# Kernel tuning notes

Hardware: AMD Instinct MI355X
Metric: run time of the kernel (lower is better)

## Reference

```python
import jax, jax.numpy as jnp
import numpy as np

# Mamba2(d_model=256, headdim=32) defaults: d_state=128, d_conv=4, expand=2, ngroups=1, chunk=256
B, CIN, L = 8, 256, 1024
D_MODEL = CIN
D_INNER = 2 * D_MODEL            # expand=2 -> 512
HEADDIM = 32
NHEADS = D_INNER // HEADDIM      # 16
D_STATE = 128
D_CONV = 4
CONV_DIM = D_INNER + 2 * D_STATE             # 768 (ngroups=1)
D_IN_PROJ = 2 * D_INNER + 2 * D_STATE + NHEADS  # 1296
GN_GROUPS = 8
CHUNK = 256
EPS = 1e-5

def setup_inputs():
    key = jax.random.key(0)
    ks = jax.random.split(key, 8)
    x = jax.random.normal(ks[0], (B, CIN, L), jnp.float32)
    W_in = jax.random.normal(ks[1], (D_IN_PROJ, D_MODEL), jnp.float32) * 0.02
    conv_w = jax.random.normal(ks[2], (CONV_DIM, D_CONV), jnp.float32) * 0.2
    conv_b = jax.random.normal(ks[3], (CONV_DIM,), jnp.float32) * 0.02
    dt = jnp.exp(jax.random.uniform(ks[4], (NHEADS,)) * (jnp.log(0.1) - jnp.log(0.001)) + jnp.log(0.001))
    dt_bias = dt + jnp.log(-jnp.expm1(-dt))   # inverse softplus
    A_log = jnp.log(jax.random.uniform(ks[5], (NHEADS,), minval=1.0, maxval=16.0))
    Dp = jnp.ones((NHEADS,), jnp.float32)
    rms_w = jnp.ones((D_INNER,), jnp.float32)
    W_out = jax.random.normal(ks[6], (D_MODEL, D_INNER), jnp.float32) * 0.02
    gn_w = jnp.ones((CIN,), jnp.float32)
    gn_b = jnp.zeros((CIN,), jnp.float32)
    return dict(x=x, W_in=W_in, conv_w=conv_w, conv_b=conv_b, dt_bias=dt_bias,
                A_log=A_log, Dp=Dp, rms_w=rms_w, W_out=W_out, gn_w=gn_w, gn_b=gn_b)

def segsum(a):
    # a: (..., T) -> (..., T, T) with sum_{j<i<=t} a_i on/below diagonal, -inf above
    T = a.shape[-1]
    cs = jnp.cumsum(a, -1)
    d = cs[..., :, None] - cs[..., None, :]
    mask = jnp.tril(jnp.ones((T, T), bool))
    return jnp.where(mask, d, -jnp.inf)

def ssd(X, A, Bm, Cm):
    # X: (b,l,h,p) already dt-scaled; A: (b,l,h) = dt*A_cont; Bm,Cm: (b,l,n) (ngroups=1)
    b, l, h, p = X.shape
    n = Bm.shape[-1]
    c = l // CHUNK
    X = X.reshape(b, c, CHUNK, h, p)
    A = A.reshape(b, c, CHUNK, h).transpose(0, 3, 1, 2)      # (b,h,c,l)
    Bm = Bm.reshape(b, c, CHUNK, n)
    Cm = Cm.reshape(b, c, CHUNK, n)
    A_cs = jnp.cumsum(A, -1)                                  # (b,h,c,l)
    Lmat = jnp.exp(segsum(A))                                 # (b,h,c,l,l)
    Y_diag = jnp.einsum('bcln,bcsn,bhcls,bcshp->bclhp', Cm, Bm, Lmat, X)
    decay_states = jnp.exp(A_cs[..., -1:] - A_cs)             # (b,h,c,l)
    states = jnp.einsum('bcln,bhcl,bclhp->bchpn', Bm, decay_states, X)
    decay_chunk = jnp.exp(segsum(jnp.pad(A_cs[..., -1], ((0, 0), (0, 0), (1, 0)))))  # (b,h,c+1,c+1)
    states = jnp.concatenate([jnp.zeros_like(states[:, :1]), states], axis=1)        # (b,c+1,h,p,n)
    prev = jnp.einsum('bhzc,bchpn->bzhpn', decay_chunk, states)[:, :-1]              # (b,c,h,p,n)
    Y_off = jnp.einsum('bcln,bchpn,bhcl->bclhp', Cm, prev, jnp.exp(A_cs))
    return (Y_diag + Y_off).reshape(b, l, h, p)

def _forward(x, W_in, conv_w, conv_b, dt_bias, A_log, Dp, rms_w, W_out, gn_w, gn_b):
    u = jnp.transpose(x, (0, 2, 1))                           # (B,L,d_model)
    zxbcdt = u @ W_in.T                                       # (B,L,1296)
    z = zxbcdt[..., :D_INNER]
    xBC = zxbcdt[..., D_INNER:D_INNER + CONV_DIM]
    dt = jax.nn.softplus(zxbcdt[..., D_INNER + CONV_DIM:] + dt_bias)  # (B,L,H)
    # causal depthwise conv1d + SiLU
    xpad = jnp.pad(xBC, ((0, 0), (D_CONV - 1, 0), (0, 0)))
    xconv = conv_b + sum(conv_w[:, k] * xpad[:, k:k + L, :] for k in range(D_CONV))
    xconv = jax.nn.silu(xconv)
    xs = xconv[..., :D_INNER].reshape(B, L, NHEADS, HEADDIM)
    Bm = xconv[..., D_INNER:D_INNER + D_STATE]
    Cm = xconv[..., D_INNER + D_STATE:]
    A = -jnp.exp(A_log)                                       # (H,)
    Y = ssd(dt[..., None] * xs, dt * A, Bm, Cm)               # (B,L,H,P)
    Y = Y + xs * Dp[None, None, :, None]
    # gated RMSNorm (norm_before_gate=False): rmsnorm(y * silu(z)) * weight
    y = Y.reshape(B, L, D_INNER) * jax.nn.silu(z)
    y = y * jax.lax.rsqrt(jnp.mean(y * y, -1, keepdims=True) + EPS) * rms_w
    out = jnp.transpose(y @ W_out.T, (0, 2, 1))               # (B,C,L)
    # GroupNorm(8, C) over (channels_per_group, L)
    og = out.reshape(B, GN_GROUPS, CIN // GN_GROUPS, L)
    mu = og.mean((2, 3), keepdims=True)
    var = og.var((2, 3), keepdims=True)
    out = ((og - mu) * jax.lax.rsqrt(var + EPS)).reshape(B, CIN, L)
    out = out * gn_w[None, :, None] + gn_b[None, :, None]
    return out * jnp.tanh(jax.nn.softplus(out))               # Mish

def reference(x, W_in, conv_w, conv_b, dt_bias, A_log, Dp, rms_w, W_out, gn_w, gn_b):
    return _forward(x, W_in, conv_w, conv_b, dt_bias, A_log, Dp, rms_w, W_out, gn_w, gn_b)
```

## Files before the change

kernel.cpp:

```cpp
#include <hip/hip_runtime.h>
#include <hip/hip_bf16.h>
#include <math.h>

#define B_ 8
#define L_ 1024
#define DM 256
#define DI 512
#define HD 32
#define NH 16
#define DS 128
#define CDIM 768
#define NZX 1280
#define CH 256
#define NC 4
#define M_ (B_*L_)
#define EPSV 1e-5f

typedef short bf16x8 __attribute__((ext_vector_type(8)));
typedef float f32x4 __attribute__((ext_vector_type(4)));

#define OFF_ZX   0
#define SZ_ZX    (M_*NZX/2)
#define OFF_XC   (OFF_ZX+SZ_ZX)
#define SZ_XC    (M_*CDIM/2)
#define OFF_DTP  (OFF_XC+SZ_XC)
#define SZ_DTP   (4*M_*NH)
#define OFF_ACS  (OFF_DTP+SZ_DTP)
#define SZ_ACS   (B_*NC*NH*CH)
#define OFF_S0   (OFF_ACS+SZ_ACS)
#define SZ_S0    (B_*NC*CH*CH/2)
#define OFF_ST   (OFF_S0+SZ_S0)
#define SZ_ST    (B_*NC*NH*HD*DS/2)
#define OFF_Y    (OFF_ST+SZ_ST)
#define SZ_Y     (M_*DI/2)
#define OFF_YNB  (OFF_Y+SZ_Y)
#define SZ_YNB   (M_*DI/2)
#define OFF_XBF  (OFF_YNB+SZ_YNB)
#define SZ_XBF   (M_*DM/2)
#define OFF_WBF  (OFF_XBF+SZ_XBF)
#define SZ_WBF   (1296*DM/2)
#define OFF_WOBF (OFF_WBF+SZ_WBF)
#define SZ_WOBF  (DM*DI/2)
#define OFF_GNP  (OFF_WOBF+SZ_WOBF)
#define SZ_GNP   (64*2)
#define OFF_BT   (OFF_GNP+SZ_GNP)
#define SZ_BT    (32*128*256/2)
#define OFF_OUTB (OFF_BT+SZ_BT)
#define SZ_OUTB  (M_*DM/2)

__device__ __forceinline__ ushort f2bf(float v) {
  __hip_bfloat16 h = __float2bfloat16(v);
  return *(ushort*)&h;
}
__device__ __forceinline__ float bf2f(ushort u) {
  return __uint_as_float(((unsigned int)u) << 16);
}
__device__ __forceinline__ float dt_load(const float* __restrict__ dtp, size_t di) {
  float s = dtp[di] + dtp[(size_t)M_*NH + di] + dtp[2*(size_t)M_*NH + di] + dtp[3*(size_t)M_*NH + di];
  return (s > 20.f) ? s : log1pf(expf(s));
}

__device__ __forceinline__ void gload16(const ushort* g, ushort* l) {
  __builtin_amdgcn_global_load_lds(
      (const __attribute__((address_space(1))) unsigned int*)g,
      (__attribute__((address_space(3))) unsigned int*)l,
      16, 0, 0);
}

__global__ __launch_bounds__(256) void k_prep(const float* __restrict__ x,
                                              const float* __restrict__ W_in,
                                              const float* __restrict__ W_out,
                                              const float* __restrict__ dt_bias,
                                              ushort* __restrict__ xbf,
                                              ushort* __restrict__ wbf,
                                              ushort* __restrict__ wobf,
                                              float2* __restrict__ gnp,
                                              float* __restrict__ dtp) {
  __shared__ float Ts[64][65];
  __shared__ float Wd[16][65];
  const int bid = blockIdx.x;
  const int t = threadIdx.x;
  if (bid < 512) {
    const int kt = bid & 3, lt2 = (bid >> 2) & 15, b = bid >> 6;
    const int k0 = kt*64, l0 = lt2*64;
    for (int i = t; i < 1024; i += 256) {
      int kk = i>>4, lw = i&15;
      float4 v = *(const float4*)&x[(size_t)b*DM*L_ + (size_t)(k0+kk)*L_ + l0 + lw*4];
      Ts[kk][lw*4+0] = v.x; Ts[kk][lw*4+1] = v.y;
      Ts[kk][lw*4+2] = v.z; Ts[kk][lw*4+3] = v.w;
    }
    for (int i = t; i < 1024; i += 256) {
      int h = i>>6, kk = i&63;
      Wd[h][kk] = W_in[(size_t)(NZX+h)*DM + k0+kk];
    }
    __syncthreads();
    for (int i = t; i < 512; i += 256) {
      int mm = i>>3, kg = i&7;
      union { ushort u[8]; uint4 q; } pk;
#pragma unroll
      for (int j = 0; j < 8; ++j) pk.u[j] = f2bf(Ts[kg*8+j][mm]);
      *(uint4*)&xbf[(size_t)(b*L_ + l0+mm)*DM + k0 + kg*8] = pk.q;
    }
    const int h = t&15, lg = t>>4;
    const float bias = (kt == 0) ? dt_bias[h] : 0.f;
#pragma unroll
    for (int c = 0; c < 4; ++c) {
      const int ll = lg + c*16;
      float acc = bias;
#pragma unroll 8
      for (int kk = 0; kk < 64; ++kk) acc += Wd[h][kk]*Ts[kk][ll];
      dtp[(size_t)kt*M_*NH + (size_t)(b*L_ + l0+ll)*NH + h] = acc;
    }
  } else if (bid < 512 + 1296) {
    int i = (bid-512)*256 + t;
    if (i < 1296*DM) wbf[i] = f2bf(W_in[i]);
  } else if (bid < 512 + 1296 + 512) {
    int i = (bid-512-1296)*256 + t;
    wobf[i] = f2bf(W_out[i]);
  } else {
    if (t < 64) gnp[t] = make_float2(0.f, 0.f);
  }
}

__global__ __launch_bounds__(256) void k_gemm_in_mfma(const ushort* __restrict__ xbf,
                                                      const ushort* __restrict__ wbf,
                                                      ushort* __restrict__ zxb) {
  __shared__ __attribute__((aligned(16))) ushort As[2][128*32];
  __shared__ __attribute__((aligned(16))) ushort Bs[2][128*32];
  const int tid = threadIdx.x;
  const int n0 = blockIdx.x*128, m0 = blockIdx.y*128;
  const int wave = tid>>6, lane = tid&63;
  const int lr = lane&15, quad = lane>>4;
  const int rA = lane>>2;
  const int cA = (lane&3)*8;
  f32x4 acc[2][8];
#pragma unroll
  for (int mi=0;mi<2;++mi)
#pragma unroll
    for (int ni=0;ni<8;++ni)
#pragma unroll
      for (int r=0;r<4;++r) acc[mi][ni][r] = 0.f;
  auto STAGE = [&](int buf, int k0) {
#pragma unroll
    for (int j = 0; j < 2; ++j) {
      const int ch = 2*wave + j;
      const int row = ch*16 + rA;
      gload16(xbf + (size_t)(m0+row)*DM + k0 + cA, &As[buf][ch*512]);
      gload16(wbf + (size_t)(n0+row)*DM + k0 + cA, &Bs[buf][ch*512]);
    }
  };
  STAGE(0, 0);
#pragma unroll
  for (int i = 0; i < 8; ++i) {
    __syncthreads();
    if (i < 7) STAGE((i+1)&1, (i+1)*32);
    const int cur = i&1;
    bf16x8 af[2], bfr[8];
    af[0] = *(const bf16x8*)&As[cur][(wave*32+lr)*32 + quad*8];
    af[1] = *(const bf16x8*)&As[cur][(wave*32+16+lr)*32 + quad*8];
#pragma unroll
    for (int ni=0;ni<8;++ni) bfr[ni] = *(const bf16x8*)&Bs[cur][(ni*16+lr)*32 + quad*8];
#pragma unroll
    for (int mi=0;mi<2;++mi)
#pragma unroll
      for (int ni=0;ni<8;++ni)
        acc[mi][ni] = __builtin_amdgcn_mfma_f32_16x16x32_bf16(af[mi], bfr[ni], acc[mi][ni], 0, 0, 0);
  }
#pragma unroll
  for (int mi=0;mi<2;++mi) {
    int m = m0 + wave*32 + mi*16 + quad*4;
#pragma unroll
    for (int ni=0;ni<8;++ni) {
      int n = n0 + ni*16 + lr;
#pragma unroll
      for (int r=0;r<4;++r) zxb[(size_t)(m+r)*NZX + n] = f2bf(acc[mi][ni][r]);
    }
  }
}

__global__ __launch_bounds__(256) void k_conv(const ushort* __restrict__ zxb,
                                              const float* __restrict__ cw,
                                              const float* __restrict__ cb,
                                              ushort* __restrict__ xcb,
                                              ushort* __restrict__ btg) {
  const int j = blockIdx.x*256 + threadIdx.x;
  const int m8 = blockIdx.y*8;
  const int l0 = m8 & 1023;
  const int mb = m8 & ~1023;
  const float4 w = *(const float4*)&cw[j*4];
  const float bias = cb[j];
  float v[11];
#pragma unroll
  for (int i = 0; i < 11; ++i) {
    int ll = l0 - 3 + i;
    v[i] = (ll >= 0) ? bf2f(zxb[(size_t)(mb+ll)*NZX + DI + j]) : 0.f;
  }
  union { ushort u[8]; uint4 q; } res;
#pragma unroll
  for (int i = 0; i < 8; ++i) {
    float a = bias + w.x*v[i] + w.y*v[i+1] + w.z*v[i+2] + w.w*v[i+3];
    a = a / (1.f + expf(-a));
    res.u[i] = f2bf(a);
    xcb[(size_t)(mb+l0+i)*CDIM + j] = res.u[i];
  }
  if (j >= DI && j < DI+DS) {
    const int n = j - DI;
    const int bc = (mb >> 10)*NC + (l0 >> 8);
    const int lc = l0 & 255;
    *(uint4*)&btg[((size_t)bc*DS + n)*CH + lc] = res.q;
  }
}

__global__ __launch_bounds__(256) void k_s0st(const ushort* __restrict__ xcb,
                                              const ushort* __restrict__ btg,
                                              const float* __restrict__ dtp,
                                              const float* __restrict__ A_log,
                                              float* __restrict__ acs_g,
                                              ushort* __restrict__ stb,
                                              ushort* __restrict__ S0b) {
  __shared__ float acs[CH];
  __shared__ ushort Xw[32][264];
  const int role = blockIdx.x;
  const int bc = blockIdx.y;
  const int base = bc*CH;
  const int t = threadIdx.x;
  const int wave = t>>6, lane = t&63, lr = lane&15, quad = lane>>4;
  if (role < 10) {
    const int lt = (role>=6) ? 3 : (role>=3) ? 2 : (role>=1) ? 1 : 0;
    const int st = role - lt*(lt+1)/2;
    const int l = lt*64 + wave*16 + lr;
    f32x4 acc[4];
#pragma unroll
    for (int nt = 0; nt < 4; ++nt)
#pragma unroll
      for (int r = 0; r < 4; ++r) acc[nt][r] = 0.f;
#pragma unroll
    for (int ks = 0; ks < 4; ++ks) {
      bf16x8 af = *(const bf16x8*)(xcb + (size_t)(base+l)*CDIM + (DI+DS) + ks*32 + quad*8);
#pragma unroll
      for (int nt = 0; nt < 4; ++nt) {
        bf16x8 bf = *(const bf16x8*)(xcb + (size_t)(base + st*64 + nt*16 + lr)*CDIM + DI + ks*32 + quad*8);
        acc[nt] = __builtin_amdgcn_mfma_f32_16x16x32_bf16(af, bf, acc[nt], 0, 0, 0);
      }
    }
    const bool diag = (lt == st);
#pragma unroll
    for (int nt = 0; nt < 4; ++nt)
#pragma unroll
      for (int r = 0; r < 4; ++r) {
        const int lrow = lt*64 + wave*16 + quad*4 + r;
        const int scol = st*64 + nt*16 + lr;
        ushort v = (!diag || scol <= lrow) ? f2bf(acc[nt][r]) : (ushort)0;
        S0b[((size_t)bc*CH + lrow)*CH + scol] = v;
      }
    return;
  }
  const int h = role - 10;
  float dt_t = dt_load(dtp, (size_t)(base+t)*NH + h);
  float An = -expf(A_log[h]);
  acs[t] = dt_t * An;
  __syncthreads();
  for (int off = 1; off < CH; off <<= 1) {
    float v = (t >= off) ? acs[t-off] : 0.f;
    __syncthreads();
    acs[t] += v;
    __syncthreads();
  }
  float alast = acs[CH-1];
  acs_g[((size_t)bc*NH + h)*CH + t] = acs[t];
  float w = expf(alast - acs[t]) * dt_t;
  {
    const ushort* xp = xcb + (size_t)(base+t)*CDIM + h*HD;
    ushort tmp[32];
    *(uint4*)&tmp[0]  = *(const uint4*)(xp);
    *(uint4*)&tmp[8]  = *(const uint4*)(xp+8);
    *(uint4*)&tmp[16] = *(const uint4*)(xp+16);
    *(uint4*)&tmp[24] = *(const uint4*)(xp+24);
#pragma unroll
    for (int p = 0; p < 32; ++p) Xw[p][t] = f2bf(bf2f(tmp[p]) * w);
  }
  __syncthreads();
  f32x4 acc2[2][2];
#pragma unroll
  for (int mt=0;mt<2;++mt)
#pragma unroll
    for (int nt=0;nt<2;++nt)
#pragma unroll
      for (int r=0;r<4;++r) acc2[mt][nt][r] = 0.f;
  const ushort* bp = btg + (size_t)bc*DS*CH;
#pragma unroll
  for (int k0 = 0; k0 < CH; k0 += 32) {
    bf16x8 a0 = *(const bf16x8*)&Xw[lr][k0 + quad*8];
    bf16x8 a1 = *(const bf16x8*)&Xw[16+lr][k0 + quad*8];
    bf16x8 b0 = *(const bf16x8*)(bp + (size_t)(wave*32 + lr)*CH + k0 + quad*8);
    bf16x8 b1 = *(const bf16x8*)(bp + (size_t)(wave*32 + 16 + lr)*CH + k0 + quad*8);
    acc2[0][0] = __builtin_amdgcn_mfma_f32_16x16x32_bf16(a0, b0, acc2[0][0], 0,0,0);
    acc2[0][1] = __builtin_amdgcn_mfma_f32_16x16x32_bf16(a0, b1, acc2[0][1], 0,0,0);
    acc2[1][0] = __builtin_amdgcn_mfma_f32_16x16x32_bf16(a1, b0, acc2[1][0], 0,0,0);
    acc2[1][1] = __builtin_amdgcn_mfma_f32_16x16x32_bf16(a1, b1, acc2[1][1], 0,0,0);
  }
  size_t sb = ((size_t)bc*NH + h)*HD*DS;
#pragma unroll
  for (int mt = 0; mt < 2; ++mt)
#pragma unroll
    for (int nt = 0; nt < 2; ++nt)
#pragma unroll
      for (int r = 0; r < 4; ++r)
        stb[sb + (size_t)(mt*16 + quad*4 + r)*DS + wave*32 + nt*16 + lr] = f2bf(acc2[mt][nt][r]);
}

__global__ __launch_bounds__(256) void k_y_mfma(const ushort* __restrict__ xcb,
    const float* __restrict__ dtp, const float* __restrict__ acs_g,
    const ushort* __restrict__ S0b, const ushort* __restrict__ stb,
    const float* __restrict__ Dp, ushort* __restrict__ Yb) {
  __shared__ ushort Xt[32][280];
  __shared__ float acs[CH];
  __shared__ float E8[CH];
  const int t = threadIdx.x;
  const int bc = blockIdx.x, h = blockIdx.y;
  const int base = bc*CH;
  const int cc = bc & 3, bc4 = bc & ~3;
  acs[t] = acs_g[((size_t)bc*NH + h)*CH + t];
  const float dts_t = dt_load(dtp, (size_t)(base+t)*NH + h);
  {
    const ushort* xp = xcb + (size_t)(base+t)*CDIM + h*HD;
    ushort tmp[32];
    *(uint4*)&tmp[0]  = *(const uint4*)(xp);
    *(uint4*)&tmp[8]  = *(const uint4*)(xp+8);
    *(uint4*)&tmp[16] = *(const uint4*)(xp+16);
    *(uint4*)&tmp[24] = *(const uint4*)(xp+24);
#pragma unroll
    for (int p = 0; p < 32; ++p) Xt[p][t] = tmp[p];
  }
  __syncthreads();
  E8[t] = expf(acs[t & ~7] - acs[t]) * dts_t;
  __syncthreads();
  const int wave = t>>6, lane = t&63, lr = lane&15, quad = lane>>4;
  f32x4 acc[4][2];
#pragma unroll
  for (int mt=0;mt<4;++mt)
#pragma unroll
    for (int nt=0;nt<2;++nt)
#pragma unroll
      for (int r=0;r<4;++r) acc[mt][nt][r] = 0.f;
  if (cc > 0) {
    float fj[3];
    {
      float cum = 0.f;
      for (int j = cc-1; j >= 0; --j) {
        fj[j] = expf(cum);
        cum += acs_g[((size_t)(bc4+j)*NH + h)*CH + (CH-1)];
      }
    }
#pragma unroll
    for (int ks = 0; ks < 4; ++ks) {
      bf16x8 bfr[2];
#pragma unroll
      for (int nt = 0; nt < 2; ++nt) {
        float P[8];
#pragma unroll
        for (int jj = 0; jj < 8; ++jj) P[jj] = 0.f;
        for (int j = 0; j < cc; ++j) {
          bf16x8 sv = *(const bf16x8*)(stb + ((size_t)(bc4+j)*NH + h)*HD*DS
                                       + (size_t)(nt*16+lr)*DS + ks*32 + quad*8);
#pragma unroll
          for (int jj = 0; jj < 8; ++jj) P[jj] += fj[j]*bf2f((ushort)sv[jj]);
        }
        bf16x8 bb;
#pragma unroll
        for (int jj = 0; jj < 8; ++jj) bb[jj] = (short)f2bf(P[jj]);
        bfr[nt] = bb;
      }
#pragma unroll
      for (int mt = 0; mt < 4; ++mt) {
        int l = wave*64 + mt*16 + lr;
        bf16x8 af = *(const bf16x8*)(xcb + (size_t)(base+l)*CDIM + (DI+DS) + ks*32 + quad*8);
        acc[mt][0] = __builtin_amdgcn_mfma_f32_16x16x32_bf16(af, bfr[0], acc[mt][0], 0,0,0);
        acc[mt][1] = __builtin_amdgcn_mfma_f32_16x16x32_bf16(af, bfr[1], acc[mt][1], 0,0,0);
      }
    }
#pragma unroll
    for (int mt = 0; mt < 4; ++mt)
#pragma unroll
      for (int r = 0; r < 4; ++r) {
        float e = expf(acs[wave*64 + mt*16 + quad*4 + r]);
        acc[mt][0][r] *= e;
        acc[mt][1][r] *= e;
      }
  }
  float al[4];
#pragma unroll
  for (int mt = 0; mt < 4; ++mt) al[mt] = acs[wave*64 + mt*16 + lr];
  const int km3 = 2*wave + 1;
  for (int ks = 0; ks <= km3; ++ks) {
    const int sq = ks*32 + quad*8;
    const float as0 = acs[sq];
    const float4 e0 = *(const float4*)&E8[sq];
    const float4 e1 = *(const float4*)&E8[sq+4];
    const bf16x8 xb0 = *(const bf16x8*)&Xt[lr][sq];
    const bf16x8 xb1 = *(const bf16x8*)&Xt[16+lr][sq];
    const float ev[8] = {e0.x,e0.y,e0.z,e0.w,e1.x,e1.y,e1.z,e1.w};
#pragma unroll
    for (int mt = 0; mt < 4; ++mt) {
      if (ks > ((wave*64 + mt*16 + 15) >> 5)) continue;
      const int l = wave*64 + mt*16 + lr;
      const bf16x8 sb = *(const bf16x8*)(S0b + ((size_t)bc*CH + l)*CH + sq);
      const float el = expf(fminf(al[mt] - as0, 0.f));
      bf16x8 mf;
#pragma unroll
      for (int j = 0; j < 8; ++j)
        mf[j] = (short)f2bf(bf2f((ushort)sb[j]) * el * ev[j]);
      acc[mt][0] = __builtin_amdgcn_mfma_f32_16x16x32_bf16(mf, xb0, acc[mt][0], 0,0,0);
      acc[mt][1] = __builtin_amdgcn_mfma_f32_16x16x32_bf16(mf, xb1, acc[mt][1], 0,0,0);
    }
  }
  const float dph = Dp[h];
#pragma unroll
  for (int mt = 0; mt < 4; ++mt) {
    const int lb = wave*64 + mt*16 + quad*4;
#pragma unroll
    for (int nt = 0; nt < 2; ++nt) {
      const int p = nt*16 + lr;
#pragma unroll
      for (int r = 0; r < 4; ++r) {
        float xv = bf2f(Xt[p][lb+r]);
        Yb[(size_t)(base+lb+r)*DI + h*HD + p] = f2bf(acc[mt][nt][r] + dph*xv);
      }
    }
  }
}

__global__ __launch_bounds__(256) void k_rms(const ushort* __restrict__ zxb,
                                             const ushort* __restrict__ Yb,
                                             const float* __restrict__ rw,
                                             ushort* __restrict__ yn) {
  const int m = blockIdx.x*4 + (threadIdx.x>>6);
  const int lane = threadIdx.x & 63;
  const int c0 = lane*8;
  bf16x8 zv = *(const bf16x8*)(zxb + (size_t)m*NZX + c0);
  bf16x8 yv = *(const bf16x8*)(Yb  + (size_t)m*DI  + c0);
  float y[8];
  float ss = 0.f;
#pragma unroll
  for (int j = 0; j < 8; ++j) {
    float z = bf2f((ushort)zv[j]);
    y[j] = bf2f((ushort)yv[j]) * z / (1.f + expf(-z));
    ss += y[j]*y[j];
  }
#pragma unroll
  for (int off = 1; off < 64; off <<= 1) ss += __shfl_xor(ss, off);
  const float inv = rsqrtf(ss * (1.f/DI) + EPSV);
  float4 w0 = *(const float4*)&rw[c0];
  float4 w1 = *(const float4*)&rw[c0+4];
  const float wv[8] = {w0.x,w0.y,w0.z,w0.w,w1.x,w1.y,w1.z,w1.w};
  union { ushort u[8]; uint4 q; } pk;
#pragma unroll
  for (int j = 0; j < 8; ++j) pk.u[j] = f2bf(y[j] * inv * wv[j]);
  *(uint4*)(yn + (size_t)m*DI + c0) = pk.q;
}

__global__ __launch_bounds__(256) void k_gemm_out_mfma(const ushort* __restrict__ ynbf,
                                                       const ushort* __restrict__ wobf,
                                                       ushort* __restrict__ outb,
                                                       float2* __restrict__ gnp) {
  __shared__ __attribute__((aligned(16))) ushort As[2][64*32];
  __shared__ __attribute__((aligned(16))) ushort Bs[2][128*32];
  __shared__ float red[4][8];
  const int tid = threadIdx.x;
  const int n0 = blockIdx.x*128, m0 = blockIdx.y*64;
  const int wave = tid>>6, lane = tid&63;
  const int lr = lane&15, quad = lane>>4;
  const int rA = lane>>2;
  const int cA = (lane&3)*8;
  f32x4 acc[8];
#pragma unroll
  for (int ni=0;ni<8;++ni)
#pragma unroll
    for (int r=0;r<4;++r) acc[ni][r] = 0.f;
  auto STAGE = [&](int buf, int k0) {
    gload16(ynbf + (size_t)(m0 + wave*16 + rA)*DI + k0 + cA, &As[buf][wave*512]);
#pragma unroll
    for (int j = 0; j < 2; ++j) {
      const int ch = 2*wave + j;
      gload16(wobf + (size_t)(n0 + ch*16 + rA)*DI + k0 + cA, &Bs[buf][ch*512]);
    }
  };
  STAGE(0, 0);
#pragma unroll
  for (int i = 0; i < 16; ++i) {
    __syncthreads();
    if (i < 15) STAGE((i+1)&1, (i+1)*32);
    const int cur = i&1;
    bf16x8 af = *(const bf16x8*)&As[cur][(wave*16+lr)*32 + quad*8];
    bf16x8 bfr[8];
#pragma unroll
    for (int ni=0;ni<8;++ni) bfr[ni] = *(const bf16x8*)&Bs[cur][(ni*16+lr)*32 + quad*8];
#pragma unroll
    for (int ni=0;ni<8;++ni)
      acc[ni] = __builtin_amdgcn_mfma_f32_16x16x32_bf16(af, bfr[ni], acc[ni], 0, 0, 0);
  }
  const int b = m0 >> 10, l0 = m0 & 1023;
  float sg[4] = {0.f,0.f,0.f,0.f}, sq2[4] = {0.f,0.f,0.f,0.f};
#pragma unroll
  for (int ni=0;ni<8;++ni) {
    int n = n0 + ni*16 + lr;
    union { ushort u[4]; uint2 q; } pk;
#pragma unroll
    for (int r=0;r<4;++r) pk.u[r] = f2bf(acc[ni][r]);
    *(uint2*)&outb[(size_t)b*DM*L_ + (size_t)n*L_ + l0 + wave*16 + quad*4] = pk.q;
    float ps = acc[ni][0]+acc[ni][1]+acc[ni][2]+acc[ni][3];
    float pq = acc[ni][0]*acc[ni][0]+acc[ni][1]*acc[ni][1]
             + acc[ni][2]*acc[ni][2]+acc[ni][3]*acc[ni][3];
    sg[ni>>1] += ps; sq2[ni>>1] += pq;
  }
#pragma unroll
  for (int g = 0; g < 4; ++g)
#pragma unroll
    for (int off = 32; off > 0; off >>= 1) {
      sg[g]  += __shfl_down(sg[g],  off);
      sq2[g] += __shfl_down(sq2[g], off);
    }
  if (lane == 0) {
#pragma unroll
    for (int g = 0; g < 4; ++g) { red[wave][g] = sg[g]; red[wave][4+g] = sq2[g]; }
  }
  __syncthreads();
  if (tid == 0) {
    int g0 = b*8 + (n0>>5);
#pragma unroll
    for (int g = 0; g < 4; ++g) {
      float S = red[0][g]+red[1][g]+red[2][g]+red[3][g];
      float Q = red[0][4+g]+red[1][4+g]+red[2][4+g]+red[3][4+g];
      atomicAdd(&gnp[g0+g].x, S);
      atomicAdd(&gnp[g0+g].y, Q);
    }
  }
}

__global__ __launch_bounds__(256) void k_gn_apply(const float2* __restrict__ gnp,
                                                  const float* __restrict__ gw,
                                                  const float* __restrict__ gb,
                                                  const ushort* __restrict__ ob,
                                                  float* __restrict__ o) {
  const int ch = blockIdx.x & 255, b = blockIdx.x >> 8;
  const int t = threadIdx.x;
  float2 p = gnp[b*8 + (ch>>5)];
  const float mean = p.x * (1.f/(32.f*L_));
  const float var  = p.y * (1.f/(32.f*L_)) - mean*mean;
  const float inv  = rsqrtf(var + EPSV);
  const float w = gw[ch], bb = gb[ch];
  size_t base = (size_t)blockIdx.x * L_;
  ushort4 v = *(const ushort4*)&ob[base + t*4];
  float r[4] = {bf2f(v.x), bf2f(v.y), bf2f(v.z), bf2f(v.w)};
#pragma unroll
  for (int j = 0; j < 4; ++j) {
    float u = (r[j] - mean) * inv * w + bb;
    float m;
    if (u > 15.f) m = u;
    else {
      float e = expf(u);
      float a = 1.f + e;
      float a2 = a*a;
      m = u * (a2 - 1.f) / (a2 + 1.f);
    }
    r[j] = m;
  }
  *(float4*)&o[base + t*4] = make_float4(r[0], r[1], r[2], r[3]);
}

extern "C" void kernel_launch(void* const* d_in, const int* in_sizes, int n_in,
                              void* d_out, int out_size, void* d_ws, size_t ws_size,
                              hipStream_t stream) {
  const float* x       = (const float*)d_in[0];
  const float* W_in    = (const float*)d_in[1];
  const float* conv_w  = (const float*)d_in[2];
  const float* conv_b  = (const float*)d_in[3];
  const float* dt_bias = (const float*)d_in[4];
  const float* A_log   = (const float*)d_in[5];
  const float* Dp      = (const float*)d_in[6];
  const float* rms_w   = (const float*)d_in[7];
  const float* W_out   = (const float*)d_in[8];
  const float* gn_w    = (const float*)d_in[9];
  const float* gn_b    = (const float*)d_in[10];
  float* out = (float*)d_out;
  float* ws  = (float*)d_ws;

  ushort* zxb   = (ushort*)(ws + OFF_ZX);
  ushort* xcb   = (ushort*)(ws + OFF_XC);
  float*  dtp   = ws + OFF_DTP;
  float*  acs   = ws + OFF_ACS;
  ushort* S0b   = (ushort*)(ws + OFF_S0);
  ushort* stb   = (ushort*)(ws + OFF_ST);
  ushort* Ybb   = (ushort*)(ws + OFF_Y);
  ushort* ynbf  = (ushort*)(ws + OFF_YNB);
  ushort* xbf   = (ushort*)(ws + OFF_XBF);
  ushort* wbf   = (ushort*)(ws + OFF_WBF);
  ushort* wobf  = (ushort*)(ws + OFF_WOBF);
  float2* gnp   = (float2*)(ws + OFF_GNP);
  ushort* btg   = (ushort*)(ws + OFF_BT);
  ushort* outb  = (ushort*)(ws + OFF_OUTB);

  k_prep         <<<dim3(512+1296+512+1), 256, 0, stream>>>(x, W_in, W_out, dt_bias,
                                                            xbf, wbf, wobf, gnp, dtp);
  k_gemm_in_mfma <<<dim3(NZX/128, M_/128), 256, 0, stream>>>(xbf, wbf, zxb);
  k_conv         <<<dim3(3, M_/8), 256, 0, stream>>>(zxb, conv_w, conv_b, xcb, btg);
  k_s0st         <<<dim3(26, B_*NC), 256, 0, stream>>>(xcb, btg, dtp, A_log, acs, stb, S0b);
  k_y_mfma       <<<dim3(B_*NC, NH), 256, 0, stream>>>(xcb, dtp, acs, S0b, stb, Dp, Ybb);
  k_rms          <<<dim3(M_/4), 256, 0, stream>>>(zxb, Ybb, rms_w, ynbf);
  k_gemm_out_mfma<<<dim3(DM/128, M_/64), 256, 0, stream>>>(ynbf, wobf, outb, gnp);
  k_gn_apply     <<<dim3(B_*DM), 256, 0, stream>>>(gnp, gn_w, gn_b, outb, out);
}
```

Baseline: 177.4 us.

## Fuse gated RMSNorm into out-projection GEMM, shuffle-based scan, prescale X in y kernel

The gated RMSNorm kernel is merged into the output-projection GEMM. Each block normalises 32 rows straight into shared memory and multiplies them by the full 256-wide W_out, which removes the round trip of the normalised activations through global memory and one launch. The chunk cumsum in k_s0st now uses a wave shuffle scan plus a cross-wave prefix instead of a barrier-heavy LDS Hillis-Steele scan. In k_y_mfma the per-position decay factor is folded into a pre-scaled copy of X, so the inner loop does one fewer multiply per element. The cost is more LDS per block, fewer blocks in the output GEMM, and slightly different bf16 rounding.

```diff
diff --git a/kernel.cpp b/kernel.cpp
--- a/kernel.cpp
+++ b/kernel.cpp
@@ -218,7 +218,7 @@
                                               float* __restrict__ acs_g,
                                               ushort* __restrict__ stb,
                                               ushort* __restrict__ S0b) {
-  __shared__ float acs[CH];
+  __shared__ float wtot[4];
   __shared__ ushort Xw[32][264];
   const int role = blockIdx.x;
   const int bc = blockIdx.y;
@@ -258,17 +258,25 @@
   const int h = role - 10;
   float dt_t = dt_load(dtp, (size_t)(base+t)*NH + h);
   float An = -expf(A_log[h]);
-  acs[t] = dt_t * An;
+  float v = dt_t * An;
+#pragma unroll
+  for (int off = 1; off < 64; off <<= 1) {
+    float u = __shfl_up(v, off);
+    if (lane >= off) v += u;
+  }
+  if (lane == 63) wtot[wave] = v;
   __syncthreads();
-  for (int off = 1; off < CH; off <<= 1) {
-    float v = (t >= off) ? acs[t-off] : 0.f;
-    __syncthreads();
-    acs[t] += v;
-    __syncthreads();
-  }
-  float alast = acs[CH-1];
-  acs_g[((size_t)bc*NH + h)*CH + t] = acs[t];
-  float w = expf(alast - acs[t]) * dt_t;
+  float pre = 0.f, tot = 0.f;
+#pragma unroll
+  for (int wj = 0; wj < 4; ++wj) {
+    float wv = wtot[wj];
+    tot += wv;
+    if (wj < wave) pre += wv;
+  }
+  const float a = v + pre;
+  const float alast = tot;
+  acs_g[((size_t)bc*NH + h)*CH + t] = a;
+  float w = expf(alast - a) * dt_t;
   {
     const ushort* xp = xcb + (size_t)(base+t)*CDIM + h*HD;
     ushort tmp[32];
@@ -314,17 +322,17 @@
     const ushort* __restrict__ S0b, const ushort* __restrict__ stb,
     const float* __restrict__ Dp, ushort* __restrict__ Yb) {
   __shared__ ushort Xt[32][280];
+  __shared__ ushort Xs[32][280];
   __shared__ float acs[CH];
-  __shared__ float E8[CH];
   const int t = threadIdx.x;
   const int bc = blockIdx.x, h = blockIdx.y;
   const int base = bc*CH;
   const int cc = bc & 3, bc4 = bc & ~3;
   acs[t] = acs_g[((size_t)bc*NH + h)*CH + t];
   const float dts_t = dt_load(dtp, (size_t)(base+t)*NH + h);
+  ushort tmp[32];
   {
     const ushort* xp = xcb + (size_t)(base+t)*CDIM + h*HD;
-    ushort tmp[32];
     *(uint4*)&tmp[0]  = *(const uint4*)(xp);
     *(uint4*)&tmp[8]  = *(const uint4*)(xp+8);
     *(uint4*)&tmp[16] = *(const uint4*)(xp+16);
@@ -333,7 +341,9 @@
     for (int p = 0; p < 32; ++p) Xt[p][t] = tmp[p];
   }
   __syncthreads();
-  E8[t] = expf(acs[t & ~7] - acs[t]) * dts_t;
+  const float e8 = expf(acs[t & ~7] - acs[t]) * dts_t;
+#pragma unroll
+  for (int p = 0; p < 32; ++p) Xs[p][t] = f2bf(bf2f(tmp[p]) * e8);
   __syncthreads();
   const int wave = t>>6, lane = t&63, lr = lane&15, quad = lane>>4;
   f32x4 acc[4][2];
@@ -395,11 +405,8 @@
   for (int ks = 0; ks <= km3; ++ks) {
     const int sq = ks*32 + quad*8;
     const float as0 = acs[sq];
-    const float4 e0 = *(const float4*)&E8[sq];
-    const float4 e1 = *(const float4*)&E8[sq+4];
-    const bf16x8 xb0 = *(const bf16x8*)&Xt[lr][sq];
-    const bf16x8 xb1 = *(const bf16x8*)&Xt[16+lr][sq];
-    const float ev[8] = {e0.x,e0.y,e0.z,e0.w,e1.x,e1.y,e1.z,e1.w};
+    const bf16x8 xb0 = *(const bf16x8*)&Xs[lr][sq];
+    const bf16x8 xb1 = *(const bf16x8*)&Xs[16+lr][sq];
 #pragma unroll
     for (int mt = 0; mt < 4; ++mt) {
       if (ks > ((wave*64 + mt*16 + 15) >> 5)) continue;
@@ -409,7 +416,7 @@
       bf16x8 mf;
 #pragma unroll
       for (int j = 0; j < 8; ++j)
-        mf[j] = (short)f2bf(bf2f((ushort)sb[j]) * el * ev[j]);
+        mf[j] = (short)f2bf(bf2f((ushort)sb[j]) * el);
       acc[mt][0] = __builtin_amdgcn_mfma_f32_16x16x32_bf16(mf, xb0, acc[mt][0], 0,0,0);
       acc[mt][1] = __builtin_amdgcn_mfma_f32_16x16x32_bf16(mf, xb1, acc[mt][1], 0,0,0);
     }
@@ -430,91 +437,100 @@
   }
 }
 
-__global__ __launch_bounds__(256) void k_rms(const ushort* __restrict__ zxb,
-                                             const ushort* __restrict__ Yb,
-                                             const float* __restrict__ rw,
-                                             ushort* __restrict__ yn) {
-  const int m = blockIdx.x*4 + (threadIdx.x>>6);
-  const int lane = threadIdx.x & 63;
-  const int c0 = lane*8;
-  bf16x8 zv = *(const bf16x8*)(zxb + (size_t)m*NZX + c0);
-  bf16x8 yv = *(const bf16x8*)(Yb  + (size_t)m*DI  + c0);
-  float y[8];
-  float ss = 0.f;
-#pragma unroll
-  for (int j = 0; j < 8; ++j) {
-    float z = bf2f((ushort)zv[j]);
-    y[j] = bf2f((ushort)yv[j]) * z / (1.f + expf(-z));
-    ss += y[j]*y[j];
-  }
-#pragma unroll
-  for (int off = 1; off < 64; off <<= 1) ss += __shfl_xor(ss, off);
-  const float inv = rsqrtf(ss * (1.f/DI) + EPSV);
-  float4 w0 = *(const float4*)&rw[c0];
-  float4 w1 = *(const float4*)&rw[c0+4];
-  const float wv[8] = {w0.x,w0.y,w0.z,w0.w,w1.x,w1.y,w1.z,w1.w};
-  union { ushort u[8]; uint4 q; } pk;
-#pragma unroll
-  for (int j = 0; j < 8; ++j) pk.u[j] = f2bf(y[j] * inv * wv[j]);
-  *(uint4*)(yn + (size_t)m*DI + c0) = pk.q;
-}
-
-__global__ __launch_bounds__(256) void k_gemm_out_mfma(const ushort* __restrict__ ynbf,
-                                                       const ushort* __restrict__ wobf,
-                                                       ushort* __restrict__ outb,
-                                                       float2* __restrict__ gnp) {
-  __shared__ __attribute__((aligned(16))) ushort As[2][64*32];
-  __shared__ __attribute__((aligned(16))) ushort Bs[2][128*32];
-  __shared__ float red[4][8];
+__global__ __launch_bounds__(256) void k_out_fused(const ushort* __restrict__ zxb,
+                                                   const ushort* __restrict__ Yb,
+                                                   const float* __restrict__ rw,
+                                                   const ushort* __restrict__ wobf,
+                                                   ushort* __restrict__ outb,
+                                                   float2* __restrict__ gnp) {
+  __shared__ __attribute__((aligned(16))) ushort As[32*520];
+  __shared__ __attribute__((aligned(16))) ushort Bs[2][256*32];
   const int tid = threadIdx.x;
-  const int n0 = blockIdx.x*128, m0 = blockIdx.y*64;
   const int wave = tid>>6, lane = tid&63;
   const int lr = lane&15, quad = lane>>4;
-  const int rA = lane>>2;
-  const int cA = (lane&3)*8;
-  f32x4 acc[8];
-#pragma unroll
-  for (int ni=0;ni<8;++ni)
-#pragma unroll
-    for (int r=0;r<4;++r) acc[ni][r] = 0.f;
+  const int m0 = blockIdx.x*32;
   auto STAGE = [&](int buf, int k0) {
-    gload16(ynbf + (size_t)(m0 + wave*16 + rA)*DI + k0 + cA, &As[buf][wave*512]);
-#pragma unroll
-    for (int j = 0; j < 2; ++j) {
-      const int ch = 2*wave + j;
-      gload16(wobf + (size_t)(n0 + ch*16 + rA)*DI + k0 + cA, &Bs[buf][ch*512]);
+#pragma unroll
+    for (int j = 0; j < 4; ++j) {
+      const int r0 = (wave*4+j)*16;
+      gload16(wobf + (size_t)(r0 + (lane>>2))*DI + k0 + (lane&3)*8, &Bs[buf][r0*32]);
     }
   };
   STAGE(0, 0);
+  {
+    const int c0 = lane*8;
+    float4 w0 = *(const float4*)&rw[c0];
+    float4 w1 = *(const float4*)&rw[c0+4];
+    const float wv[8] = {w0.x,w0.y,w0.z,w0.w,w1.x,w1.y,w1.z,w1.w};
+    bf16x8 zv[8], yv[8];
+#pragma unroll
+    for (int i = 0; i < 8; ++i) {
+      const int m = m0 + wave*8 + i;
+      zv[i] = *(const bf16x8*)(zxb + (size_t)m*NZX + c0);
+      yv[i] = *(const bf16x8*)(Yb  + (size_t)m*DI  + c0);
+    }
+#pragma unroll
+    for (int i = 0; i < 8; ++i) {
+      float y[8]; float ss = 0.f;
+#pragma unroll
+      for (int j = 0; j < 8; ++j) {
+        float z = bf2f((ushort)zv[i][j]);
+        y[j] = bf2f((ushort)yv[i][j]) * z / (1.f + expf(-z));
+        ss += y[j]*y[j];
+      }
+#pragma unroll
+      for (int off = 1; off < 64; off <<= 1) ss += __shfl_xor(ss, off);
+      const float inv = rsqrtf(ss * (1.f/DI) + EPSV);
+      union { ushort u[8]; uint4 q; } pk;
+#pragma unroll
+      for (int j = 0; j < 8; ++j) pk.u[j] = f2bf(y[j] * inv * wv[j]);
+      *(uint4*)&As[(wave*8+i)*520 + c0] = pk.q;
+    }
+  }
+  f32x4 acc[2][4];
+#pragma unroll
+  for (int mf=0;mf<2;++mf)
+#pragma unroll
+    for (int nt=0;nt<4;++nt)
+#pragma unroll
+      for (int r=0;r<4;++r) acc[mf][nt][r] = 0.f;
 #pragma unroll
   for (int i = 0; i < 16; ++i) {
     __syncthreads();
     if (i < 15) STAGE((i+1)&1, (i+1)*32);
     const int cur = i&1;
-    bf16x8 af = *(const bf16x8*)&As[cur][(wave*16+lr)*32 + quad*8];
-    bf16x8 bfr[8];
-#pragma unroll
-    for (int ni=0;ni<8;++ni) bfr[ni] = *(const bf16x8*)&Bs[cur][(ni*16+lr)*32 + quad*8];
-#pragma unroll
-    for (int ni=0;ni<8;++ni)
-      acc[ni] = __builtin_amdgcn_mfma_f32_16x16x32_bf16(af, bfr[ni], acc[ni], 0, 0, 0);
+    bf16x8 af[2], bfr[4];
+#pragma unroll
+    for (int mf = 0; mf < 2; ++mf)
+      af[mf] = *(const bf16x8*)&As[(mf*16+lr)*520 + i*32 + quad*8];
+#pragma unroll
+    for (int nt = 0; nt < 4; ++nt)
+      bfr[nt] = *(const bf16x8*)&Bs[cur][(wave*64 + nt*16 + lr)*32 + quad*8];
+#pragma unroll
+    for (int mf = 0; mf < 2; ++mf)
+#pragma unroll
+      for (int nt = 0; nt < 4; ++nt)
+        acc[mf][nt] = __builtin_amdgcn_mfma_f32_16x16x32_bf16(af[mf], bfr[nt], acc[mf][nt], 0, 0, 0);
   }
   const int b = m0 >> 10, l0 = m0 & 1023;
-  float sg[4] = {0.f,0.f,0.f,0.f}, sq2[4] = {0.f,0.f,0.f,0.f};
-#pragma unroll
-  for (int ni=0;ni<8;++ni) {
-    int n = n0 + ni*16 + lr;
-    union { ushort u[4]; uint2 q; } pk;
-#pragma unroll
-    for (int r=0;r<4;++r) pk.u[r] = f2bf(acc[ni][r]);
-    *(uint2*)&outb[(size_t)b*DM*L_ + (size_t)n*L_ + l0 + wave*16 + quad*4] = pk.q;
-    float ps = acc[ni][0]+acc[ni][1]+acc[ni][2]+acc[ni][3];
-    float pq = acc[ni][0]*acc[ni][0]+acc[ni][1]*acc[ni][1]
-             + acc[ni][2]*acc[ni][2]+acc[ni][3]*acc[ni][3];
-    sg[ni>>1] += ps; sq2[ni>>1] += pq;
-  }
-#pragma unroll
-  for (int g = 0; g < 4; ++g)
+  float sg[2] = {0.f,0.f}, sq2[2] = {0.f,0.f};
+#pragma unroll
+  for (int nt = 0; nt < 4; ++nt) {
+    const int n = wave*64 + nt*16 + lr;
+#pragma unroll
+    for (int mf = 0; mf < 2; ++mf) {
+      union { ushort u[4]; uint2 q; } pk;
+#pragma unroll
+      for (int r=0;r<4;++r) pk.u[r] = f2bf(acc[mf][nt][r]);
+      *(uint2*)&outb[(size_t)b*DM*L_ + (size_t)n*L_ + l0 + mf*16 + quad*4] = pk.q;
+      float ps = acc[mf][nt][0]+acc[mf][nt][1]+acc[mf][nt][2]+acc[mf][nt][3];
+      float pq = acc[mf][nt][0]*acc[mf][nt][0]+acc[mf][nt][1]*acc[mf][nt][1]
+               + acc[mf][nt][2]*acc[mf][nt][2]+acc[mf][nt][3]*acc[mf][nt][3];
+      sg[nt>>1] += ps; sq2[nt>>1] += pq;
+    }
+  }
+#pragma unroll
+  for (int g = 0; g < 2; ++g)
 #pragma unroll
     for (int off = 32; off > 0; off >>= 1) {
       sg[g]  += __shfl_down(sg[g],  off);
@@ -522,17 +538,9 @@
     }
   if (lane == 0) {
 #pragma unroll
-    for (int g = 0; g < 4; ++g) { red[wave][g] = sg[g]; red[wave][4+g] = sq2[g]; }
-  }
-  __syncthreads();
-  if (tid == 0) {
-    int g0 = b*8 + (n0>>5);
-#pragma unroll
-    for (int g = 0; g < 4; ++g) {
-      float S = red[0][g]+red[1][g]+red[2][g]+red[3][g];
-      float Q = red[0][4+g]+red[1][4+g]+red[2][4+g]+red[3][4+g];
-      atomicAdd(&gnp[g0+g].x, S);
-      atomicAdd(&gnp[g0+g].y, Q);
+    for (int g = 0; g < 2; ++g) {
+      atomicAdd(&gnp[b*8 + wave*2 + g].x, sg[g]);
+      atomicAdd(&gnp[b*8 + wave*2 + g].y, sq2[g]);
     }
   }
 }
@@ -592,7 +600,6 @@
   ushort* S0b   = (ushort*)(ws + OFF_S0);
   ushort* stb   = (ushort*)(ws + OFF_ST);
   ushort* Ybb   = (ushort*)(ws + OFF_Y);
-  ushort* ynbf  = (ushort*)(ws + OFF_YNB);
   ushort* xbf   = (ushort*)(ws + OFF_XBF);
   ushort* wbf   = (ushort*)(ws + OFF_WBF);
   ushort* wobf  = (ushort*)(ws + OFF_WOBF);
@@ -606,7 +613,6 @@
   k_conv         <<<dim3(3, M_/8), 256, 0, stream>>>(zxb, conv_w, conv_b, xcb, btg);
   k_s0st         <<<dim3(26, B_*NC), 256, 0, stream>>>(xcb, btg, dtp, A_log, acs, stb, S0b);
   k_y_mfma       <<<dim3(B_*NC, NH), 256, 0, stream>>>(xcb, dtp, acs, S0b, stb, Dp, Ybb);
-  k_rms          <<<dim3(M_/4), 256, 0, stream>>>(zxb, Ybb, rms_w, ynbf);
-  k_gemm_out_mfma<<<dim3(DM/128, M_/64), 256, 0, stream>>>(ynbf, wobf, outb, gnp);
+  k_out_fused    <<<dim3(M_/32), 256, 0, stream>>>(zxb, Ybb, rms_w, wobf, outb, gnp);
   k_gn_apply     <<<dim3(B_*DM), 256, 0, stream>>>(gnp, gn_w, gn_b, outb, out);
 }
```

Result: no change. 180.3 us (+1.7%).

## Factor SSD decay into running rescale; use wave-shuffle scan for cumsum

Applied to the files above, without the earlier changes.

The chunk-local cumsum in k_s0st now uses a warp shuffle scan plus per-wave totals, replacing the shared-memory Hillis-Steele loop and its many barriers. In k_y_mfma the decay matrix is no longer applied elementwise to each S0 tile before the MFMA. Instead the inputs are prescaled by exp(acs[32-block start] - acs), the accumulators are rescaled by a per-block factor g as the loop walks the k-blocks, and the final row factor is applied in the epilogue. Row tiles are interleaved across waves to balance the causal triangle work. This removes per-element exp and bf16 conversion in the inner loop, but makes the accumulated values depend on ratios of exponentials that could lose precision for large decays.

```diff
diff --git a/kernel.cpp b/kernel.cpp
--- a/kernel.cpp
+++ b/kernel.cpp
@@ -218,7 +218,7 @@
                                               float* __restrict__ acs_g,
                                               ushort* __restrict__ stb,
                                               ushort* __restrict__ S0b) {
-  __shared__ float acs[CH];
+  __shared__ float wtot[4];
   __shared__ ushort Xw[32][264];
   const int role = blockIdx.x;
   const int bc = blockIdx.y;
@@ -258,17 +258,25 @@
   const int h = role - 10;
   float dt_t = dt_load(dtp, (size_t)(base+t)*NH + h);
   float An = -expf(A_log[h]);
-  acs[t] = dt_t * An;
+  float v = dt_t * An;
+#pragma unroll
+  for (int off = 1; off < 64; off <<= 1) {
+    float u = __shfl_up(v, off);
+    if (lane >= off) v += u;
+  }
+  if (lane == 63) wtot[wave] = v;
   __syncthreads();
-  for (int off = 1; off < CH; off <<= 1) {
-    float v = (t >= off) ? acs[t-off] : 0.f;
-    __syncthreads();
-    acs[t] += v;
-    __syncthreads();
-  }
-  float alast = acs[CH-1];
-  acs_g[((size_t)bc*NH + h)*CH + t] = acs[t];
-  float w = expf(alast - acs[t]) * dt_t;
+  float pre = 0.f, tot = 0.f;
+#pragma unroll
+  for (int wj = 0; wj < 4; ++wj) {
+    float wv = wtot[wj];
+    tot += wv;
+    if (wj < wave) pre += wv;
+  }
+  const float a = v + pre;
+  const float alast = tot;
+  acs_g[((size_t)bc*NH + h)*CH + t] = a;
+  float w = expf(alast - a) * dt_t;
   {
     const ushort* xp = xcb + (size_t)(base+t)*CDIM + h*HD;
     ushort tmp[32];
@@ -314,17 +322,17 @@
     const ushort* __restrict__ S0b, const ushort* __restrict__ stb,
     const float* __restrict__ Dp, ushort* __restrict__ Yb) {
   __shared__ ushort Xt[32][280];
+  __shared__ ushort Xs[32][280];
   __shared__ float acs[CH];
-  __shared__ float E8[CH];
   const int t = threadIdx.x;
   const int bc = blockIdx.x, h = blockIdx.y;
   const int base = bc*CH;
   const int cc = bc & 3, bc4 = bc & ~3;
   acs[t] = acs_g[((size_t)bc*NH + h)*CH + t];
   const float dts_t = dt_load(dtp, (size_t)(base+t)*NH + h);
+  ushort tmp[32];
   {
     const ushort* xp = xcb + (size_t)(base+t)*CDIM + h*HD;
-    ushort tmp[32];
     *(uint4*)&tmp[0]  = *(const uint4*)(xp);
     *(uint4*)&tmp[8]  = *(const uint4*)(xp+8);
     *(uint4*)&tmp[16] = *(const uint4*)(xp+16);
@@ -333,7 +341,9 @@
     for (int p = 0; p < 32; ++p) Xt[p][t] = tmp[p];
   }
   __syncthreads();
-  E8[t] = expf(acs[t & ~7] - acs[t]) * dts_t;
+  const float e32 = expf(acs[t & ~31] - acs[t]) * dts_t;
+#pragma unroll
+  for (int p = 0; p < 32; ++p) Xs[p][t] = f2bf(bf2f(tmp[p]) * e32);
   __syncthreads();
   const int wave = t>>6, lane = t&63, lr = lane&15, quad = lane>>4;
   f32x4 acc[4][2];
@@ -373,58 +383,54 @@
       }
 #pragma unroll
       for (int mt = 0; mt < 4; ++mt) {
-        int l = wave*64 + mt*16 + lr;
+        int l = mt*64 + wave*16 + lr;
         bf16x8 af = *(const bf16x8*)(xcb + (size_t)(base+l)*CDIM + (DI+DS) + ks*32 + quad*8);
         acc[mt][0] = __builtin_amdgcn_mfma_f32_16x16x32_bf16(af, bfr[0], acc[mt][0], 0,0,0);
         acc[mt][1] = __builtin_amdgcn_mfma_f32_16x16x32_bf16(af, bfr[1], acc[mt][1], 0,0,0);
       }
     }
+    const float es0 = expf(acs[0]);
 #pragma unroll
     for (int mt = 0; mt < 4; ++mt)
 #pragma unroll
-      for (int r = 0; r < 4; ++r) {
-        float e = expf(acs[wave*64 + mt*16 + quad*4 + r]);
-        acc[mt][0][r] *= e;
-        acc[mt][1][r] *= e;
+      for (int nt = 0; nt < 2; ++nt)
+#pragma unroll
+        for (int r = 0; r < 4; ++r) acc[mt][nt][r] *= es0;
+  }
+  const int Kw = (12 + wave) >> 1;
+  for (int ks = 0; ks <= Kw; ++ks) {
+    const int sq = ks*32;
+    const bf16x8 xb0 = *(const bf16x8*)&Xs[lr][sq + quad*8];
+    const bf16x8 xb1 = *(const bf16x8*)&Xs[16+lr][sq + quad*8];
+    const float g = (ks > 0) ? expf(acs[sq] - acs[sq-32]) : 1.f;
+#pragma unroll
+    for (int mt = 0; mt < 4; ++mt) {
+      const int rt = 4*mt + wave;
+      if (ks > (rt>>1)) continue;
+      if (ks > 0) {
+#pragma unroll
+        for (int r = 0; r < 4; ++r) { acc[mt][0][r] *= g; acc[mt][1][r] *= g; }
       }
-  }
-  float al[4];
-#pragma unroll
-  for (int mt = 0; mt < 4; ++mt) al[mt] = acs[wave*64 + mt*16 + lr];
-  const int km3 = 2*wave + 1;
-  for (int ks = 0; ks <= km3; ++ks) {
-    const int sq = ks*32 + quad*8;
-    const float as0 = acs[sq];
-    const float4 e0 = *(const float4*)&E8[sq];
-    const float4 e1 = *(const float4*)&E8[sq+4];
-    const bf16x8 xb0 = *(const bf16x8*)&Xt[lr][sq];
-    const bf16x8 xb1 = *(const bf16x8*)&Xt[16+lr][sq];
-    const float ev[8] = {e0.x,e0.y,e0.z,e0.w,e1.x,e1.y,e1.z,e1.w};
-#pragma unroll
-    for (int mt = 0; mt < 4; ++mt) {
-      if (ks > ((wave*64 + mt*16 + 15) >> 5)) continue;
-      const int l = wave*64 + mt*16 + lr;
-      const bf16x8 sb = *(const bf16x8*)(S0b + ((size_t)bc*CH + l)*CH + sq);
-      const float el = expf(fminf(al[mt] - as0, 0.f));
-      bf16x8 mf;
-#pragma unroll
-      for (int j = 0; j < 8; ++j)
-        mf[j] = (short)f2bf(bf2f((ushort)sb[j]) * el * ev[j]);
-      acc[mt][0] = __builtin_amdgcn_mfma_f32_16x16x32_bf16(mf, xb0, acc[mt][0], 0,0,0);
-      acc[mt][1] = __builtin_amdgcn_mfma_f32_16x16x32_bf16(mf, xb1, acc[mt][1], 0,0,0);
+      const int l = mt*64 + wave*16 + lr;
+      const bf16x8 sb = *(const bf16x8*)(S0b + ((size_t)bc*CH + l)*CH + sq + quad*8);
+      acc[mt][0] = __builtin_amdgcn_mfma_f32_16x16x32_bf16(sb, xb0, acc[mt][0], 0,0,0);
+      acc[mt][1] = __builtin_amdgcn_mfma_f32_16x16x32_bf16(sb, xb1, acc[mt][1], 0,0,0);
     }
   }
   const float dph = Dp[h];
 #pragma unroll
   for (int mt = 0; mt < 4; ++mt) {
-    const int lb = wave*64 + mt*16 + quad*4;
-#pragma unroll
-    for (int nt = 0; nt < 2; ++nt) {
-      const int p = nt*16 + lr;
-#pragma unroll
-      for (int r = 0; r < 4; ++r) {
+    const int Kmt = (4*mt + wave) >> 1;
+    const float aref = acs[32*Kmt];
+    const int lb = mt*64 + wave*16 + quad*4;
+#pragma unroll
+    for (int r = 0; r < 4; ++r) {
+      const float e = expf(acs[lb+r] - aref);
+#pragma unroll
+      for (int nt = 0; nt < 2; ++nt) {
+        const int p = nt*16 + lr;
         float xv = bf2f(Xt[p][lb+r]);
-        Yb[(size_t)(base+lb+r)*DI + h*HD + p] = f2bf(acc[mt][nt][r] + dph*xv);
+        Yb[(size_t)(base+lb+r)*DI + h*HD + p] = f2bf(acc[mt][nt][r]*e + dph*xv);
       }
     }
   }
```

After: 176.0 us. About the same (-0.8%).
